# Performance work log

Hardware: AMD Instinct MI355X
Metric: run time of the kernel (lower is better)

The kernel has to match this reference:

```python
import jax, jax.numpy as jnp
import numpy as np

NUM_HEADS = 16

def setup_inputs() -> dict:
    key = jax.random.key(0)
    k1, k2, k3 = jax.random.split(key, 3)
    B, N, D = 4, 2048, 1024
    init_attn_std = D ** (-0.5)
    x = jax.random.normal(k1, (B, N, D), dtype=jnp.float32)
    qkv_w = jax.random.normal(k2, (D, 3 * D), dtype=jnp.float32) * init_attn_std
    proj_w = jax.random.normal(k3, (D, D), dtype=jnp.float32) * init_attn_std
    proj_b = jnp.zeros((D,), dtype=jnp.float32)
    return {"x": x, "qkv_w": qkv_w, "proj_w": proj_w, "proj_b": proj_b}

def reference(x, qkv_w, proj_w, proj_b):
    B, N, D = x.shape
    H = NUM_HEADS
    hd = D // H
    scale = hd ** (-0.5)
    # QKV projection (no bias, qkv_bias=False)
    qkv = (x @ qkv_w).reshape(B, N, 3, H, hd)
    q, k, v = jnp.moveaxis(qkv, 2, 0)  # each [B, N, H, hd]
    # scaled dot-product attention with causal mask (matches flax nn.dot_product_attention)
    scores = jnp.einsum('bqhd,bkhd->bhqk', q * scale, k)  # [B, H, N, N]
    causal = jnp.tril(jnp.ones((N, N), dtype=bool))
    big_neg = jnp.finfo(scores.dtype).min
    scores = jnp.where(causal, scores, big_neg)
    attn = jax.nn.softmax(scores, axis=-1)
    out = jnp.einsum('bhqk,bkhd->bqhd', attn, v).reshape(B, N, D)
    # output projection (proj_bias=True)
    return out @ proj_w + proj_b
```

## Files before the change

### kernel.cpp

```cpp
#include <hip/hip_runtime.h>

typedef __attribute__((ext_vector_type(8))) short sh8;
typedef __attribute__((ext_vector_type(8))) __bf16 bf8v;
typedef __attribute__((ext_vector_type(4))) float f4v;
typedef __attribute__((ext_vector_type(16))) float f16v;
typedef __attribute__((ext_vector_type(4))) unsigned u4v;

__device__ __forceinline__ float fast_exp2(float x) { return __builtin_amdgcn_exp2f(x); }

__device__ __forceinline__ unsigned short f2bf(float f) {
  unsigned u = __builtin_bit_cast(unsigned, f);
  u += 0x7fffu + ((u >> 16) & 1u);
  return (unsigned short)(u >> 16);
}
__device__ __forceinline__ float bf2f(unsigned short h) {
  unsigned u = ((unsigned)h) << 16;
  return __builtin_bit_cast(float, u);
}

__device__ __forceinline__ void glds16(const unsigned short* g, unsigned short* l) {
  __builtin_amdgcn_global_load_lds((const __attribute__((address_space(1))) void*)g,
                                   (__attribute__((address_space(3))) void*)l, 16, 0, 0);
}

__global__ __launch_bounds__(256) void cast_kernel(const float* __restrict__ in,
                                                   unsigned short* __restrict__ out) {
  const int idx = (blockIdx.x * 256 + threadIdx.x) * 4;
  const float4 v = *(const float4*)(in + idx);
  ushort4 o;
  o.x = f2bf(v.x); o.y = f2bf(v.y); o.z = f2bf(v.z); o.w = f2bf(v.w);
  *(ushort4*)(out + idx) = o;
}

__global__ __launch_bounds__(256) void transpose_cast_kernel(const float* __restrict__ in,
                                                             unsigned short* __restrict__ out,
                                                             int R, int C) {
  __shared__ float tile[32][33];
  const int c0 = blockIdx.x * 32, r0 = blockIdx.y * 32;
  const int tx = threadIdx.x, ty = threadIdx.y;
#pragma unroll
  for (int i = 0; i < 4; ++i)
    tile[ty + 8 * i][tx] = in[(size_t)(r0 + ty + 8 * i) * C + c0 + tx];
  __syncthreads();
#pragma unroll
  for (int i = 0; i < 4; ++i)
    out[(size_t)(c0 + ty + 8 * i) * R + r0 + tx] = f2bf(tile[tx][ty + 8 * i]);
}

template <int MODE>
__global__ __launch_bounds__(256, 4) void gemm_bf16_kernel(
    const unsigned short* __restrict__ A,
    const unsigned short* __restrict__ Bt,
    int M, int N, int K,
    unsigned short* __restrict__ q_out, unsigned short* __restrict__ k_out,
    unsigned short* __restrict__ v_out,
    const float* __restrict__ bias, float* __restrict__ c_out) {
  __shared__ alignas(16) unsigned short smem[128 * 128];
  unsigned short* As = smem;
  unsigned short* Bs = smem + 4096;
  const int tid = threadIdx.x;
  const int lane = tid & 63;
  const int wave = tid >> 6;
  const int wr = (wave >> 1) * 64;
  const int wc = (wave & 1) * 64;
  const int bm = blockIdx.x * 128;
  const int bn = blockIdx.y * 128;
  const int fr = lane & 15;
  const int kq = lane >> 4;

  f4v acc[4][4] = {};

  const int r16 = lane >> 2;
  const int srcsl = (lane & 3) ^ ((r16 >> 1) & 3);
  const int rb0 = wave * 32, rb1 = wave * 32 + 16;

  const int rsl = (kq ^ ((fr >> 1) & 3)) * 8;
  const int nT = K >> 5;

  for (int j = 0; j < nT; ++j) {
    const int k0 = j * 32;
    __syncthreads();
    glds16(&A[(size_t)(bm + rb0 + r16) * K + k0 + srcsl * 8], &As[rb0 * 32]);
    glds16(&A[(size_t)(bm + rb1 + r16) * K + k0 + srcsl * 8], &As[rb1 * 32]);
    glds16(&Bt[(size_t)(bn + rb0 + r16) * K + k0 + srcsl * 8], &Bs[rb0 * 32]);
    glds16(&Bt[(size_t)(bn + rb1 + r16) * K + k0 + srcsl * 8], &Bs[rb1 * 32]);
    __syncthreads();

    bf8v af[4], bfv[4];
#pragma unroll
    for (int m = 0; m < 4; ++m)
      af[m] = __builtin_bit_cast(bf8v, *(const sh8*)&As[(wr + m * 16 + fr) * 32 + rsl]);
#pragma unroll
    for (int n = 0; n < 4; ++n)
      bfv[n] = __builtin_bit_cast(bf8v, *(const sh8*)&Bs[(wc + n * 16 + fr) * 32 + rsl]);
    __builtin_amdgcn_s_setprio(1);
#pragma unroll
    for (int m = 0; m < 4; ++m)
#pragma unroll
      for (int n = 0; n < 4; ++n)
        acc[m][n] = __builtin_amdgcn_mfma_f32_16x16x32_bf16(af[m], bfv[n], acc[m][n], 0, 0, 0);
    __builtin_amdgcn_s_setprio(0);
  }

  if (MODE == 0 && blockIdx.y >= 16) {
    unsigned short* Vlds = smem;
    __syncthreads();
#pragma unroll
    for (int m = 0; m < 4; ++m)
#pragma unroll
      for (int n = 0; n < 4; ++n)
#pragma unroll
        for (int i = 0; i < 4; ++i) {
          const int rp = wr + m * 16 + kq * 4 + i;
          const int cp = wc + n * 16 + fr;
          Vlds[cp * 128 + (((rp >> 3) ^ (cp & 7)) << 3) + (rp & 7)] = f2bf(acc[m][n][i]);
        }
    __syncthreads();
    const int cp = tid >> 1, half = tid & 1;
    const int b = bm >> 11;
    const int h = ((bn - 2048) >> 6) + (cp >> 6);
    const int d = cp & 63;
    unsigned short* dst =
        v_out + ((size_t)((b * 16 + h) * 64 + d)) * 2048 + (bm & 2047) + half * 64;
#pragma unroll
    for (int s = 0; s < 8; ++s) {
      const int slot = (half * 8 + s) ^ (cp & 7);
      *(sh8*)(dst + s * 8) = *(const sh8*)&Vlds[cp * 128 + slot * 8];
    }
    return;
  }

#pragma unroll
  for (int m = 0; m < 4; ++m) {
#pragma unroll
    for (int n = 0; n < 4; ++n) {
#pragma unroll
      for (int i = 0; i < 4; ++i) {
        const int r = bm + wr + m * 16 + kq * 4 + i;
        const int c = bn + wc + n * 16 + fr;
        const float val = acc[m][n][i];
        if (MODE == 0) {
          const int b = r >> 11, nidx = r & 2047;
          const int rem = c & 1023;
          const int h = rem >> 6, d = rem & 63;
          const size_t off = ((size_t)((b * 16 + h) * 2048 + nidx)) * 64 + d;
          if (blockIdx.y < 8) q_out[off] = f2bf(val * 0.18033688f);
          else                k_out[off] = f2bf(val);
        } else {
          c_out[(size_t)r * N + c] = val + bias[c];
        }
      }
    }
  }
}

__global__ __launch_bounds__(256, 2) void attn_kernel(
    const unsigned short* __restrict__ Q, const unsigned short* __restrict__ Kg,
    const unsigned short* __restrict__ Vtg, unsigned short* __restrict__ O) {
  __shared__ alignas(16) unsigned short Ks[4][64 * 64];
  __shared__ alignas(16) unsigned short Vts[4][64 * 64];
  const int tid = threadIdx.x;
  const int lane = tid & 63;
  const int w = tid >> 6;
  const int q31 = lane & 31, hi = lane >> 5;
  const int sw = (lane & 7) << 3;
  const int wg = (blockIdx.x & 7) * 64 + (blockIdx.x >> 3);
  const int bh = wg >> 3;
  const int pair = wg & 7;
  const int qtA = pair, qtB = 15 - pair;
  const unsigned short* Qb = Q + (size_t)bh * (2048 * 64);
  const unsigned short* Kb = Kg + (size_t)bh * (2048 * 64);
  const unsigned short* Vtb = Vtg + (size_t)bh * (64 * 2048);
  const int q0wA = qtA * 128 + w * 32;
  const int q0wB = qtB * 128 + w * 32;

  bf8v qfA[4], qfB[4];
#pragma unroll
  for (int dk = 0; dk < 4; ++dk) {
    qfA[dk] = __builtin_bit_cast(bf8v, *(const sh8*)&Qb[(size_t)(q0wA + q31) * 64 + 8 * hi + 16 * dk]);
    qfB[dk] = __builtin_bit_cast(bf8v, *(const sh8*)&Qb[(size_t)(q0wB + q31) * 64 + 8 * hi + 16 * dk]);
  }

  f16v oA0 = {}, oA1 = {}, oB0 = {}, oB1 = {};
  float mA = -1e30f, lA = 0.f, mB = -1e30f, lB = 0.f;

  const int r8 = lane >> 3;
  const int gslot = (lane & 7) ^ r8;
  const int rb0 = w * 16, rb1 = w * 16 + 8;

#define STAGE(g)                                                                              \
  {                                                                                           \
    const int _b = (g) & 3;                                                                   \
    glds16(&Kb[(size_t)((g) * 64 + rb0 + r8) * 64 + gslot * 8], &Ks[_b][rb0 * 64]);           \
    glds16(&Kb[(size_t)((g) * 64 + rb1 + r8) * 64 + gslot * 8], &Ks[_b][rb1 * 64]);           \
    glds16(&Vtb[(size_t)(rb0 + r8) * 2048 + (g) * 64 + gslot * 8], &Vts[_b][rb0 * 64]);       \
    glds16(&Vtb[(size_t)(rb1 + r8) * 2048 + (g) * 64 + gslot * 8], &Vts[_b][rb1 * 64]);       \
  }

  auto body = [&](int j, int buf, int q0w, bf8v (&qf)[4], f16v& o0, f16v& o1,
                  float& m_i, float& l_i) {
    f16v s0 = {}, s1 = {};
    __builtin_amdgcn_s_setprio(1);
#pragma unroll
    for (int dk = 0; dk < 4; ++dk) {
      const int col = (8 * hi + 16 * dk) ^ sw;
      const bf8v k0 = __builtin_bit_cast(bf8v, *(const sh8*)&Ks[buf][q31 * 64 + col]);
      const bf8v k1 = __builtin_bit_cast(bf8v, *(const sh8*)&Ks[buf][(32 + q31) * 64 + col]);
      s0 = __builtin_amdgcn_mfma_f32_32x32x16_bf16(k0, qf[dk], s0, 0, 0, 0);
      s1 = __builtin_amdgcn_mfma_f32_32x32x16_bf16(k1, qf[dk], s1, 0, 0, 0);
    }
    __builtin_amdgcn_s_setprio(0);

    const int qg = q0w + q31;
    if (j * 64 + 63 > q0w) {
#pragma unroll
      for (int r = 0; r < 16; ++r) {
        const int kl = j * 64 + (r & 3) + 8 * (r >> 2) + 4 * hi;
        if (kl > qg) s0[r] = -1e30f;
        if (kl + 32 > qg) s1[r] = -1e30f;
      }
    }

    float mx = -1e30f;
#pragma unroll
    for (int r = 0; r < 16; ++r) mx = fmaxf(mx, fmaxf(s0[r], s1[r]));
    mx = fmaxf(mx, __shfl_xor(mx, 32));

    if (!__all(mx - m_i <= 8.f)) {
      const float mn = fmaxf(m_i, mx);
      const float alpha = fast_exp2(m_i - mn);
      m_i = mn;
      l_i *= alpha;
#pragma unroll
      for (int r = 0; r < 16; ++r) {
        const float ar = __shfl(alpha, (r & 3) + 8 * (r >> 2) + 4 * hi);
        o0[r] *= ar;
        o1[r] *= ar;
      }
    }

    float ps = 0.f;
#pragma unroll
    for (int r = 0; r < 16; ++r) {
      s0[r] = fast_exp2(s0[r] - m_i);
      s1[r] = fast_exp2(s1[r] - m_i);
      ps += s0[r] + s1[r];
    }
    ps += __shfl_xor(ps, 32);
    l_i += ps;

    unsigned w0[8], w1[8];
#pragma unroll
    for (int jj = 0; jj < 8; ++jj) {
      asm("v_cvt_pk_bf16_f32 %0, %1, %2" : "=v"(w0[jj]) : "v"(s0[2 * jj]), "v"(s0[2 * jj + 1]));
      asm("v_cvt_pk_bf16_f32 %0, %1, %2" : "=v"(w1[jj]) : "v"(s1[2 * jj]), "v"(s1[2 * jj + 1]));
    }

#pragma unroll
    for (int ks = 0; ks < 4; ++ks) {
      const int j0 = 4 * (ks & 1);
      unsigned x0 = (ks < 2 ? w0[j0 + 0] : w1[j0 + 0]);
      unsigned y0 = (ks < 2 ? w0[j0 + 2] : w1[j0 + 2]);
      unsigned x1 = (ks < 2 ? w0[j0 + 1] : w1[j0 + 1]);
      unsigned y1 = (ks < 2 ? w0[j0 + 3] : w1[j0 + 3]);
      asm("v_permlane32_swap_b32 %0, %1" : "+v"(x0), "+v"(y0));
      asm("v_permlane32_swap_b32 %0, %1" : "+v"(x1), "+v"(y1));
      u4v pw;
      pw[0] = x0; pw[1] = x1; pw[2] = y0; pw[3] = y1;
      const bf8v pa = __builtin_bit_cast(bf8v, pw);

      const int colv = (8 * hi + 16 * ks) ^ sw;
      const bf8v vf0 = __builtin_bit_cast(bf8v, *(const sh8*)&Vts[buf][q31 * 64 + colv]);
      const bf8v vf1 = __builtin_bit_cast(bf8v, *(const sh8*)&Vts[buf][(32 + q31) * 64 + colv]);
      __builtin_amdgcn_s_setprio(1);
      o0 = __builtin_amdgcn_mfma_f32_32x32x16_bf16(pa, vf0, o0, 0, 0, 0);
      o1 = __builtin_amdgcn_mfma_f32_32x32x16_bf16(pa, vf1, o1, 0, 0, 0);
      __builtin_amdgcn_s_setprio(0);
    }
  };

  const int b = bh >> 4, h = bh & 15;
  auto epi = [&](int q0w, f16v& o0, f16v& o1, float l_i) {
    const float rl = 1.f / l_i;
#pragma unroll
    for (int r = 0; r < 16; ++r) {
      const int cr = (r & 3) + 8 * (r >> 2) + 4 * hi;
      const float lr = __shfl(rl, cr);
      const size_t base = ((size_t)(b * 2048 + q0w + cr)) * 1024 + h * 64 + q31;
      O[base] = f2bf(o0[r] * lr);
      O[base + 32] = f2bf(o1[r] * lr);
    }
  };

  const int nA = 2 * qtA + 2;
  const int nT = 2 * qtB + 2;

  STAGE(0);
  STAGE(1);

  for (int j = 0; j < nT; ++j) {
    const int buf = j & 3;
    if (j + 2 < nT) {
      STAGE(j + 2);
      asm volatile("s_waitcnt vmcnt(8)" ::: "memory");
    } else if (j + 1 < nT) {
      asm volatile("s_waitcnt vmcnt(4)" ::: "memory");
    } else {
      asm volatile("s_waitcnt vmcnt(0)" ::: "memory");
    }
    __builtin_amdgcn_s_barrier();

    if (j < nA) body(j, buf, q0wA, qfA, oA0, oA1, mA, lA);
    body(j, buf, q0wB, qfB, oB0, oB1, mB, lB);

    if (j == nA - 1) epi(q0wA, oA0, oA1, lA);
  }
#undef STAGE

  epi(q0wB, oB0, oB1, lB);
}

extern "C" void kernel_launch(void* const* d_in, const int* in_sizes, int n_in,
                              void* d_out, int out_size, void* d_ws, size_t ws_size,
                              hipStream_t stream) {
  const float* x      = (const float*)d_in[0];
  const float* qkv_w  = (const float*)d_in[1];
  const float* proj_w = (const float*)d_in[2];
  const float* proj_b = (const float*)d_in[3];
  float* out = (float*)d_out;

  unsigned short* ws = (unsigned short*)d_ws;
  const size_t NE = (size_t)8192 * 1024;
  unsigned short* xb     = ws;
  unsigned short* wqkvT  = xb + NE;
  unsigned short* wprojT = wqkvT + (size_t)3072 * 1024;
  unsigned short* qb     = wprojT + (size_t)1024 * 1024;
  unsigned short* kb     = qb + NE;
  unsigned short* vt     = kb + NE;
  unsigned short* ab     = xb;

  cast_kernel<<<8192, 256, 0, stream>>>(x, xb);
  transpose_cast_kernel<<<dim3(96, 32), dim3(32, 8), 0, stream>>>(qkv_w, wqkvT, 1024, 3072);
  transpose_cast_kernel<<<dim3(32, 32), dim3(32, 8), 0, stream>>>(proj_w, wprojT, 1024, 1024);

  gemm_bf16_kernel<0><<<dim3(64, 24), 256, 0, stream>>>(
      xb, wqkvT, 8192, 3072, 1024, qb, kb, vt, nullptr, nullptr);

  attn_kernel<<<512, 256, 0, stream>>>(qb, kb, vt, ab);

  gemm_bf16_kernel<1><<<dim3(64, 8), 256, 0, stream>>>(
      ab, wprojT, 8192, 1024, 1024, nullptr, nullptr, nullptr, proj_b, out);
}
```

Measured before the change: 174.1 us.

## Multi-buffer output-projection GEMM with async LDS prefetch two stages ahead

For the output projection GEMM (MODE 1), replaces the single-buffered load/sync/compute loop with a 4-slot LDS ring. Global-to-LDS loads are issued two K-steps ahead and synchronised with vmcnt waits plus a single barrier, so memory latency can overlap MFMA work. This needs 64KB of LDS, so the occupancy hint drops to 2 blocks per SM for this mode. The QKV GEMM path is unchanged.

```diff
diff --git a/kernel.cpp b/kernel.cpp
--- a/kernel.cpp
+++ b/kernel.cpp
@@ -48,16 +48,15 @@
 }
 
 template <int MODE>
-__global__ __launch_bounds__(256, 4) void gemm_bf16_kernel(
+__global__ __launch_bounds__(256, MODE == 0 ? 4 : 2) void gemm_bf16_kernel(
     const unsigned short* __restrict__ A,
     const unsigned short* __restrict__ Bt,
     int M, int N, int K,
     unsigned short* __restrict__ q_out, unsigned short* __restrict__ k_out,
     unsigned short* __restrict__ v_out,
     const float* __restrict__ bias, float* __restrict__ c_out) {
-  __shared__ alignas(16) unsigned short smem[128 * 128];
-  unsigned short* As = smem;
-  unsigned short* Bs = smem + 4096;
+  constexpr int SMEM_SH = (MODE == 0) ? (128 * 128) : (2 * 4 * 128 * 32);
+  __shared__ alignas(16) unsigned short smem[SMEM_SH];
   const int tid = threadIdx.x;
   const int lane = tid & 63;
   const int wave = tid >> 6;
@@ -73,84 +72,134 @@
   const int r16 = lane >> 2;
   const int srcsl = (lane & 3) ^ ((r16 >> 1) & 3);
   const int rb0 = wave * 32, rb1 = wave * 32 + 16;
-
   const int rsl = (kq ^ ((fr >> 1) & 3)) * 8;
   const int nT = K >> 5;
 
-  for (int j = 0; j < nT; ++j) {
-    const int k0 = j * 32;
-    __syncthreads();
-    glds16(&A[(size_t)(bm + rb0 + r16) * K + k0 + srcsl * 8], &As[rb0 * 32]);
-    glds16(&A[(size_t)(bm + rb1 + r16) * K + k0 + srcsl * 8], &As[rb1 * 32]);
-    glds16(&Bt[(size_t)(bn + rb0 + r16) * K + k0 + srcsl * 8], &Bs[rb0 * 32]);
-    glds16(&Bt[(size_t)(bn + rb1 + r16) * K + k0 + srcsl * 8], &Bs[rb1 * 32]);
-    __syncthreads();
-
-    bf8v af[4], bfv[4];
+  if constexpr (MODE == 0) {
+    unsigned short* As = smem;
+    unsigned short* Bs = smem + 4096;
+    for (int j = 0; j < nT; ++j) {
+      const int k0 = j * 32;
+      __syncthreads();
+      glds16(&A[(size_t)(bm + rb0 + r16) * K + k0 + srcsl * 8], &As[rb0 * 32]);
+      glds16(&A[(size_t)(bm + rb1 + r16) * K + k0 + srcsl * 8], &As[rb1 * 32]);
+      glds16(&Bt[(size_t)(bn + rb0 + r16) * K + k0 + srcsl * 8], &Bs[rb0 * 32]);
+      glds16(&Bt[(size_t)(bn + rb1 + r16) * K + k0 + srcsl * 8], &Bs[rb1 * 32]);
+      __syncthreads();
+
+      bf8v af[4], bfv[4];
+#pragma unroll
+      for (int m = 0; m < 4; ++m)
+        af[m] = __builtin_bit_cast(bf8v, *(const sh8*)&As[(wr + m * 16 + fr) * 32 + rsl]);
+#pragma unroll
+      for (int n = 0; n < 4; ++n)
+        bfv[n] = __builtin_bit_cast(bf8v, *(const sh8*)&Bs[(wc + n * 16 + fr) * 32 + rsl]);
+      __builtin_amdgcn_s_setprio(1);
+#pragma unroll
+      for (int m = 0; m < 4; ++m)
+#pragma unroll
+        for (int n = 0; n < 4; ++n)
+          acc[m][n] = __builtin_amdgcn_mfma_f32_16x16x32_bf16(af[m], bfv[n], acc[m][n], 0, 0, 0);
+      __builtin_amdgcn_s_setprio(0);
+    }
+
+    if (blockIdx.y >= 16) {
+      unsigned short* Vlds = smem;
+      __syncthreads();
+#pragma unroll
+      for (int m = 0; m < 4; ++m)
+#pragma unroll
+        for (int n = 0; n < 4; ++n)
+#pragma unroll
+          for (int i = 0; i < 4; ++i) {
+            const int rp = wr + m * 16 + kq * 4 + i;
+            const int cp = wc + n * 16 + fr;
+            Vlds[cp * 128 + (((rp >> 3) ^ (cp & 7)) << 3) + (rp & 7)] = f2bf(acc[m][n][i]);
+          }
+      __syncthreads();
+      const int cp = tid >> 1, half = tid & 1;
+      const int b = bm >> 11;
+      const int h = ((bn - 2048) >> 6) + (cp >> 6);
+      const int d = cp & 63;
+      unsigned short* dst =
+          v_out + ((size_t)((b * 16 + h) * 64 + d)) * 2048 + (bm & 2047) + half * 64;
+#pragma unroll
+      for (int s = 0; s < 8; ++s) {
+        const int slot = (half * 8 + s) ^ (cp & 7);
+        *(sh8*)(dst + s * 8) = *(const sh8*)&Vlds[cp * 128 + slot * 8];
+      }
+      return;
+    }
+
 #pragma unroll
     for (int m = 0; m < 4; ++m)
-      af[m] = __builtin_bit_cast(bf8v, *(const sh8*)&As[(wr + m * 16 + fr) * 32 + rsl]);
-#pragma unroll
-    for (int n = 0; n < 4; ++n)
-      bfv[n] = __builtin_bit_cast(bf8v, *(const sh8*)&Bs[(wc + n * 16 + fr) * 32 + rsl]);
-    __builtin_amdgcn_s_setprio(1);
-#pragma unroll
-    for (int m = 0; m < 4; ++m)
 #pragma unroll
       for (int n = 0; n < 4; ++n)
-        acc[m][n] = __builtin_amdgcn_mfma_f32_16x16x32_bf16(af[m], bfv[n], acc[m][n], 0, 0, 0);
-    __builtin_amdgcn_s_setprio(0);
-  }
-
-  if (MODE == 0 && blockIdx.y >= 16) {
-    unsigned short* Vlds = smem;
-    __syncthreads();
-#pragma unroll
-    for (int m = 0; m < 4; ++m)
-#pragma unroll
-      for (int n = 0; n < 4; ++n)
 #pragma unroll
         for (int i = 0; i < 4; ++i) {
-          const int rp = wr + m * 16 + kq * 4 + i;
-          const int cp = wc + n * 16 + fr;
-          Vlds[cp * 128 + (((rp >> 3) ^ (cp & 7)) << 3) + (rp & 7)] = f2bf(acc[m][n][i]);
-        }
-    __syncthreads();
-    const int cp = tid >> 1, half = tid & 1;
-    const int b = bm >> 11;
-    const int h = ((bn - 2048) >> 6) + (cp >> 6);
-    const int d = cp & 63;
-    unsigned short* dst =
-        v_out + ((size_t)((b * 16 + h) * 64 + d)) * 2048 + (bm & 2047) + half * 64;
-#pragma unroll
-    for (int s = 0; s < 8; ++s) {
-      const int slot = (half * 8 + s) ^ (cp & 7);
-      *(sh8*)(dst + s * 8) = *(const sh8*)&Vlds[cp * 128 + slot * 8];
-    }
-    return;
-  }
-
-#pragma unroll
-  for (int m = 0; m < 4; ++m) {
-#pragma unroll
-    for (int n = 0; n < 4; ++n) {
-#pragma unroll
-      for (int i = 0; i < 4; ++i) {
-        const int r = bm + wr + m * 16 + kq * 4 + i;
-        const int c = bn + wc + n * 16 + fr;
-        const float val = acc[m][n][i];
-        if (MODE == 0) {
+          const int r = bm + wr + m * 16 + kq * 4 + i;
+          const int c = bn + wc + n * 16 + fr;
+          const float val = acc[m][n][i];
           const int b = r >> 11, nidx = r & 2047;
           const int rem = c & 1023;
           const int h = rem >> 6, d = rem & 63;
           const size_t off = ((size_t)((b * 16 + h) * 2048 + nidx)) * 64 + d;
           if (blockIdx.y < 8) q_out[off] = f2bf(val * 0.18033688f);
           else                k_out[off] = f2bf(val);
-        } else {
-          c_out[(size_t)r * N + c] = val + bias[c];
         }
+  } else {
+    unsigned short* As = smem;
+    unsigned short* Bs = smem + 16384;
+#define GSTAGE(g)                                                                            \
+    {                                                                                        \
+      const int _b = ((g) & 3) * 4096;                                                       \
+      const int _k0 = (g) * 32;                                                              \
+      glds16(&A[(size_t)(bm + rb0 + r16) * K + _k0 + srcsl * 8], &As[_b + rb0 * 32]);        \
+      glds16(&A[(size_t)(bm + rb1 + r16) * K + _k0 + srcsl * 8], &As[_b + rb1 * 32]);        \
+      glds16(&Bt[(size_t)(bn + rb0 + r16) * K + _k0 + srcsl * 8], &Bs[_b + rb0 * 32]);       \
+      glds16(&Bt[(size_t)(bn + rb1 + r16) * K + _k0 + srcsl * 8], &Bs[_b + rb1 * 32]);       \
+    }
+    GSTAGE(0);
+    GSTAGE(1);
+    for (int j = 0; j < nT; ++j) {
+      const int buf = (j & 3) * 4096;
+      if (j + 2 < nT) {
+        GSTAGE(j + 2);
+        asm volatile("s_waitcnt vmcnt(8)" ::: "memory");
+      } else if (j + 1 < nT) {
+        asm volatile("s_waitcnt vmcnt(4)" ::: "memory");
+      } else {
+        asm volatile("s_waitcnt vmcnt(0)" ::: "memory");
       }
-    }
+      __builtin_amdgcn_s_barrier();
+
+      bf8v af[4], bfv[4];
+#pragma unroll
+      for (int m = 0; m < 4; ++m)
+        af[m] = __builtin_bit_cast(bf8v, *(const sh8*)&As[buf + (wr + m * 16 + fr) * 32 + rsl]);
+#pragma unroll
+      for (int n = 0; n < 4; ++n)
+        bfv[n] = __builtin_bit_cast(bf8v, *(const sh8*)&Bs[buf + (wc + n * 16 + fr) * 32 + rsl]);
+      __builtin_amdgcn_s_setprio(1);
+#pragma unroll
+      for (int m = 0; m < 4; ++m)
+#pragma unroll
+        for (int n = 0; n < 4; ++n)
+          acc[m][n] = __builtin_amdgcn_mfma_f32_16x16x32_bf16(af[m], bfv[n], acc[m][n], 0, 0, 0);
+      __builtin_amdgcn_s_setprio(0);
+    }
+#undef GSTAGE
+
+#pragma unroll
+    for (int m = 0; m < 4; ++m)
+#pragma unroll
+      for (int n = 0; n < 4; ++n)
+#pragma unroll
+        for (int i = 0; i < 4; ++i) {
+          const int r = bm + wr + m * 16 + kq * 4 + i;
+          const int c = bn + wc + n * 16 + fr;
+          c_out[(size_t)r * N + c] = acc[m][n][i] + bias[c];
+        }
   }
 }
 
```

New measurement: 172.0 us. No clear change (-1.2%).
